# Performance work log

Measured on AMD Instinct MI355X. Metric: run time of the kernel, lower is better.

## Reference

```python
import jax, jax.numpy as jnp
import numpy as np

L, D, H, DH, DI, V, S, B = 12, 768, 12, 64, 3072, 32000, 512, 2
LN_EPS = 1e-3  # keras LayerNormalization default epsilon

def _gelu(x):
    return x * 0.5 * (1.0 + jnp.tanh(np.sqrt(2.0 / np.pi).astype(np.float32) * (x + 0.044715 * x ** 3)))

def _layer_norm(x, g, b):
    mu = jnp.mean(x, axis=-1, keepdims=True)
    var = jnp.mean((x - mu) ** 2, axis=-1, keepdims=True)
    return (x - mu) * jax.lax.rsqrt(var + LN_EPS) * g + b

def _rel_shift(x, klen):
    # x: [qlen, rlen, b, n] -> shifted [qlen, klen, b, n]
    q, r, b, n = x.shape
    x = x.reshape(r, q, b, n)[1:].reshape(q, r - 1, b, n)
    return x[:, :klen]

def _pos_emb():
    # relative positions klen..-qlen+1 (attn_type='bi', mems=None -> klen=qlen=S)
    pos_seq = jnp.arange(S, -S, -1.0, dtype=jnp.float32)                      # [2S]
    inv_freq = 1.0 / (10000.0 ** (jnp.arange(0, D, 2, dtype=jnp.float32) / D))
    sinusoid = pos_seq[:, None] * inv_freq[None, :]
    pe = jnp.concatenate([jnp.sin(sinusoid), jnp.cos(sinusoid)], axis=-1)     # [2S, D]
    return jnp.broadcast_to(pe[:, None, :], (2 * S, B, D))                    # [2S, B, D]

def setup_inputs() -> dict:
    key = jax.random.key(0)
    ks = jax.random.split(key, 12)
    rn = lambda k, sh: 0.02 * jax.random.normal(k, sh, dtype=jnp.float32)
    return {
        "inp_k": jax.random.randint(ks[0], (S, B), 0, V),
        "seg_ids": jax.random.randint(ks[1], (S, B), 0, 2),
        "input_mask": jax.random.randint(ks[2], (S, B), 0, 2),
        "lookup_table": rn(ks[3], (V, D)),
        "Wq": rn(ks[4], (L, D, H, DH)),
        "Wk": rn(ks[5], (L, D, H, DH)),
        "Wv": rn(ks[6], (L, D, H, DH)),
        "Wr": rn(ks[7], (L, D, H, DH)),
        "Wo": rn(ks[8], (L, D, H, DH)),
        "r_w_bias": rn(ks[9], (L, H, DH)),
        "r_r_bias": rn(ks[10], (L, H, DH)),
        "r_s_bias": rn(ks[11], (L, H, DH)),
        "seg_embed": rn(jax.random.fold_in(key, 100), (L, 2, H, DH)),
        "ln_attn_g": jnp.ones((L, D), jnp.float32),
        "ln_attn_b": jnp.zeros((L, D), jnp.float32),
        "ln_ff_g": jnp.ones((L, D), jnp.float32),
        "ln_ff_b": jnp.zeros((L, D), jnp.float32),
        "ff_w1": rn(jax.random.fold_in(key, 101), (L, D, DI)),
        "ff_b1": jnp.zeros((L, DI), jnp.float32),
        "ff_w2": rn(jax.random.fold_in(key, 102), (L, DI, D)),
        "ff_b2": jnp.zeros((L, D), jnp.float32),
    }

def reference(inp_k, seg_ids, input_mask, lookup_table, Wq, Wk, Wv, Wr, Wo,
              r_w_bias, r_r_bias, r_s_bias, seg_embed,
              ln_attn_g, ln_attn_b, ln_ff_g, ln_ff_b,
              ff_w1, ff_b1, ff_w2, ff_b2):
    h = lookup_table[inp_k]                                                   # [S,B,D]
    r = _pos_emb()                                                            # [2S,B,D]
    # segment "same/different" one-hot matrix [q,k,b,2]
    seg_mat = jax.nn.one_hot((seg_ids[:, None, :] != seg_ids[None, :, :]).astype(jnp.int32), 2, dtype=jnp.float32)
    attn_mask = input_mask.astype(jnp.float32)[None, :, :, None]              # [1,S,B,1] broadcast over q,heads
    scale = DH ** -0.5
    for l in range(L):
        q = jnp.einsum('ibh,hnd->ibnd', h, Wq[l])
        k = jnp.einsum('ibh,hnd->ibnd', h, Wk[l])
        v = jnp.einsum('ibh,hnd->ibnd', h, Wv[l])
        kr = jnp.einsum('ibh,hnd->ibnd', r, Wr[l])                            # [2S,B,n,d]
        ac = jnp.einsum('ibnd,jbnd->ijbn', q + r_w_bias[l], k)
        bd = _rel_shift(jnp.einsum('ibnd,jbnd->ijbn', q + r_r_bias[l], kr), S)
        ef = jnp.einsum('ibnd,snd->ibns', q + r_s_bias[l], seg_embed[l])
        ef = jnp.einsum('ijbs,ibns->ijbn', seg_mat, ef)
        score = (ac + bd + ef) * scale - 1e30 * attn_mask
        prob = jax.nn.softmax(score, axis=1)                                  # softmax over key axis j
        vec = jnp.einsum('ijbn,jbnd->ibnd', prob, v)
        h = _layer_norm(jnp.einsum('ibnd,hnd->ibh', vec, Wo[l]) + h, ln_attn_g[l], ln_attn_b[l])
        ff = _gelu(jnp.einsum('ibd,df->ibf', h, ff_w1[l]) + ff_b1[l])
        ff = jnp.einsum('ibf,fd->ibd', ff, ff_w2[l]) + ff_b2[l]
        h = _layer_norm(ff + h, ln_ff_g[l], ln_ff_b[l])
    return h
```

## Files before the change

kernel.cpp:

```cpp
#include <hip/hip_runtime.h>
#include <hip/hip_bf16.h>
#include <math.h>

#define S 512
#define B 2
#define D 768
#define H 12
#define DH 64
#define DI 3072
#define NL 12
#define NTOK (S * B)

typedef __attribute__((ext_vector_type(8))) short short8v;
typedef __attribute__((ext_vector_type(4))) float f32x4;

__device__ __forceinline__ unsigned short f2b(float f) {
  union { float f; unsigned int u; } v; v.f = f;
  unsigned int r = v.u + 0x7fffu + ((v.u >> 16) & 1u);
  return (unsigned short)(r >> 16);
}
__device__ __forceinline__ float b2f(unsigned short u) {
  union { unsigned int u; float f; } v; v.u = ((unsigned int)u) << 16;
  return v.f;
}

__device__ __forceinline__ float gelu_f(float x) {
  const float c = 0.7978845608028654f;
  float t = tanhf(c * (x + 0.044715f * x * x * x));
  return x * 0.5f * (1.0f + t);
}

__device__ __forceinline__ int vkey(int r) {
  return ((((r & 7) ^ ((r >> 3) & 7)) & 7) << 3);
}

__global__ __launch_bounds__(256) void embed_kernel(const int* __restrict__ inp_k,
                                                    const float* __restrict__ lut,
                                                    float* __restrict__ h,
                                                    unsigned short* __restrict__ h_bf) {
  int t = blockIdx.x;
  int id = inp_k[t];
  for (int j = threadIdx.x; j < D; j += 256) {
    float v = lut[(size_t)id * D + j];
    h[t * D + j] = v;
    h_bf[t * D + j] = f2b(v);
  }
}

__global__ __launch_bounds__(384) void posemb_kernel(unsigned short* __restrict__ r2b) {
  int j = blockIdx.x;
  int d = threadIdx.x;
  float pos = (float)(S - j);
  float inv_freq = expf(-logf(10000.0f) * (2.0f * (float)d / (float)D));
  float x = pos * inv_freq;
  r2b[j * D + d]       = f2b(sinf(x));
  r2b[j * D + 384 + d] = f2b(cosf(x));
}

__device__ __forceinline__ void transpose_swz(const float* __restrict__ src,
                                              unsigned short* __restrict__ dst,
                                              int K, int N, int tile, int n_base,
                                              float* __restrict__ Ls ) {
  int ntk = K >> 6;
  int tk = tile % ntk, tn = tile / ntk;
  int k0 = tk << 6, n0 = tn << 6;
  int tid = threadIdx.x;
  int rr = tid >> 4, c4 = (tid & 15) * 4;
#pragma unroll
  for (int r = 0; r < 4; ++r) {
    int k = rr + r * 16;
    float4 a = *(const float4*)&src[(size_t)(k0 + k) * N + n0 + c4];
    Ls[(c4 + 0) * 65 + k] = a.x;
    Ls[(c4 + 1) * 65 + k] = a.y;
    Ls[(c4 + 2) * 65 + k] = a.z;
    Ls[(c4 + 3) * 65 + k] = a.w;
  }
  __syncthreads();
  int nl = tid >> 2, kc0 = (tid & 3) << 4;
  float f[16];
#pragma unroll
  for (int c = 0; c < 16; ++c) f[c] = Ls[nl * 65 + kc0 + c];
  short8v v0, v1;
#pragma unroll
  for (int e = 0; e < 8; ++e) {
    v0[e] = (short)f2b(f[e]);
    v1[e] = (short)f2b(f[8 + e]);
  }
  int ng = n_base + n0;
  size_t tilebase = ((size_t)(ng >> 7) * ntk + tk) * 8192;
  int row = (ng & 64) + nl;
  int key = (row & 7) << 3;
  *(short8v*)&dst[tilebase + row * 64 + (kc0 ^ key)] = v0;
  *(short8v*)&dst[tilebase + row * 64 + ((kc0 + 8) ^ key)] = v1;
}

__global__ __launch_bounds__(256) void prep_all(const float* __restrict__ Wq,
                                                const float* __restrict__ Wk,
                                                const float* __restrict__ Wv,
                                                const float* __restrict__ Wr,
                                                const float* __restrict__ Wo,
                                                const float* __restrict__ W1,
                                                const float* __restrict__ W2,
                                                unsigned short* __restrict__ wqkv_t,
                                                unsigned short* __restrict__ wr_t,
                                                unsigned short* __restrict__ wo_t,
                                                unsigned short* __restrict__ w1_t,
                                                unsigned short* __restrict__ w2_t) {
  __shared__ float Ls[64 * 65];
  const size_t DD = (size_t)D * D;
  const size_t DDI = (size_t)D * DI;
  int tb = blockIdx.x;
  int l = tb / 1872, t2 = tb % 1872;
  int tid = threadIdx.x;
  if (t2 < 432) {
    int which = t2 / 144, tile = t2 % 144;
    const float* src = (which == 0 ? Wq : (which == 1 ? Wk : Wv)) + l * DD;
    transpose_swz(src, wqkv_t + l * 3 * DD, D, D, tile, which * D, Ls);
  } else if (t2 < 576) {
    transpose_swz(Wr + l * DD, wr_t + l * DD, D, D, t2 - 432, 0, Ls);
  } else if (t2 < 1152) {
    transpose_swz(W1 + l * DDI, w1_t + l * DDI, D, DI, t2 - 576, 0, Ls);
  } else if (t2 < 1728) {
    transpose_swz(W2 + l * DDI, w2_t + l * DDI, DI, D, t2 - 1152, 0, Ls);
  } else {
    int c = t2 - 1728;
    int tkk = c % 12, tnn = c / 12;
    int k0 = tkk << 6, n0 = tnn << 6;
    int nl = tid >> 2, kc0 = (tid & 3) << 4;
    const float* srcp = Wo + l * DD + (size_t)(n0 + nl) * D + k0 + kc0;
    float4 a0 = *(const float4*)&srcp[0];
    float4 a1 = *(const float4*)&srcp[4];
    float4 a2 = *(const float4*)&srcp[8];
    float4 a3 = *(const float4*)&srcp[12];
    short8v v0, v1;
    v0[0] = (short)f2b(a0.x); v0[1] = (short)f2b(a0.y); v0[2] = (short)f2b(a0.z); v0[3] = (short)f2b(a0.w);
    v0[4] = (short)f2b(a1.x); v0[5] = (short)f2b(a1.y); v0[6] = (short)f2b(a1.z); v0[7] = (short)f2b(a1.w);
    v1[0] = (short)f2b(a2.x); v1[1] = (short)f2b(a2.y); v1[2] = (short)f2b(a2.z); v1[3] = (short)f2b(a2.w);
    v1[4] = (short)f2b(a3.x); v1[5] = (short)f2b(a3.y); v1[6] = (short)f2b(a3.z); v1[7] = (short)f2b(a3.w);
    unsigned short* dst = wo_t + l * DD;
    size_t tilebase = ((size_t)(n0 >> 7) * 12 + tkk) * 8192;
    int row = (n0 & 64) + nl;
    int key = (row & 7) << 3;
    *(short8v*)&dst[tilebase + row * 64 + (kc0 ^ key)] = v0;
    *(short8v*)&dst[tilebase + row * 64 + ((kc0 + 8) ^ key)] = v1;
  }
}

template <int ACT, int OUTBF>
__device__ __forceinline__ void gemm_tile(const unsigned short* __restrict__ A,
                                          const unsigned short* __restrict__ Wt,
                                          const float* __restrict__ bias,
                                          float* __restrict__ Cf,
                                          unsigned short* __restrict__ Cb,
                                          int N, int K, int bm, int bn,
                                          int kbeg, int kend) {
  __shared__ __align__(16) unsigned short As[64 * 64];
  __shared__ __align__(16) unsigned short Bs[128 * 64];
  const int tid = threadIdx.x, lane = tid & 63, w = tid >> 6;
  const int l8 = lane >> 3, lm8 = lane & 7;
  const int aColByte = ((lm8 ^ l8) << 4);
  const int KT = K >> 6;
  const size_t wtn = (size_t)(bn >> 7) * KT;

  f32x4 acc[4][2];
#pragma unroll
  for (int mi = 0; mi < 4; ++mi)
#pragma unroll
    for (int ni = 0; ni < 2; ++ni)
      acc[mi][ni] = (f32x4){0.f, 0.f, 0.f, 0.f};

  for (int kt = kbeg; kt < kend; kt += 64) {
    __syncthreads();
#pragma unroll
    for (int c = 0; c < 2; ++c) {
      int row = c * 32 + w * 8 + l8;
      const char* src = (const char*)&A[(size_t)(bm + row) * K + kt] + aColByte;
      __builtin_amdgcn_global_load_lds(
          (const __attribute__((address_space(1))) void*)src,
          (__attribute__((address_space(3))) void*)((char*)As + c * 4096 + w * 1024),
          16, 0, 0);
    }
    const char* wt = (const char*)&Wt[(wtn + (kt >> 6)) * 8192];
#pragma unroll
    for (int c = 0; c < 4; ++c) {
      __builtin_amdgcn_global_load_lds(
          (const __attribute__((address_space(1))) void*)(wt + c * 4096 + w * 1024 + lane * 16),
          (__attribute__((address_space(3))) void*)((char*)Bs + c * 4096 + w * 1024),
          16, 0, 0);
    }
    __syncthreads();
#pragma unroll
    for (int ks = 0; ks < 2; ++ks) {
      const int kus = ks * 32 + (lane >> 4) * 8;
      short8v af[4], bf[2];
#pragma unroll
      for (int mi = 0; mi < 4; ++mi) {
        int row = mi * 16 + (lane & 15);
        af[mi] = *(const short8v*)&As[row * 64 + (kus ^ ((row & 7) << 3))];
      }
#pragma unroll
      for (int ni = 0; ni < 2; ++ni) {
        int row = w * 32 + ni * 16 + (lane & 15);
        bf[ni] = *(const short8v*)&Bs[row * 64 + (kus ^ ((row & 7) << 3))];
      }
#pragma unroll
      for (int mi = 0; mi < 4; ++mi)
#pragma unroll
        for (int ni = 0; ni < 2; ++ni)
          acc[mi][ni] = __builtin_amdgcn_mfma_f32_16x16x32_bf16(af[mi], bf[ni], acc[mi][ni], 0, 0, 0);
    }
  }

  int r0 = (lane >> 4) * 4, cc = lane & 15;
#pragma unroll
  for (int mi = 0; mi < 4; ++mi) {
    int row = bm + mi * 16 + r0;
#pragma unroll
    for (int ni = 0; ni < 2; ++ni) {
      int col = bn + w * 32 + ni * 16 + cc;
      float bv = bias ? bias[col] : 0.0f;
#pragma unroll
      for (int r = 0; r < 4; ++r) {
        float v = acc[mi][ni][r] + bv;
        if (ACT == 1) v = gelu_f(v);
        if (OUTBF) Cb[(size_t)(row + r) * N + col] = f2b(v);
        else       Cf[(size_t)(row + r) * N + col] = v;
      }
    }
  }
}

__global__ __launch_bounds__(256) void gemm_qkv(const unsigned short* __restrict__ h_bf,
                                                const unsigned short* __restrict__ wqkv,
                                                unsigned short* __restrict__ qkv_bf) {
  int bx = blockIdx.x;
  gemm_tile<0, 1>(h_bf, wqkv, nullptr, nullptr, qkv_bf, 2304, 768,
                  (bx / 18) * 64, (bx % 18) * 128, 0, 768);
}

__global__ __launch_bounds__(256) void gemm_kr_all(const unsigned short* __restrict__ r2_bf,
                                                   const unsigned short* __restrict__ wr_t,
                                                   unsigned short* __restrict__ kr_all) {
  int bx = blockIdx.x;
  int l = bx / 96, b2 = bx % 96;
  gemm_tile<0, 1>(r2_bf, wr_t + (size_t)l * D * D, nullptr, nullptr,
                  kr_all + (size_t)l * NTOK * D, 768, 768,
                  (b2 / 6) * 64, (b2 % 6) * 128, 0, 768);
}

template <int ACT>
__global__ __launch_bounds__(256) void gemm_bias(const unsigned short* __restrict__ A,
                                                 const unsigned short* __restrict__ W,
                                                 const float* __restrict__ bias,
                                                 unsigned short* __restrict__ C,
                                                 int N, int K, int ncb) {
  int bx = blockIdx.x;
  gemm_tile<ACT, 1>(A, W, bias, nullptr, C, N, K, (bx / ncb) * 64, (bx % ncb) * 128, 0, K);
}

__global__ __launch_bounds__(256) void gemm_splitk(const unsigned short* __restrict__ A,
                                                   const unsigned short* __restrict__ W,
                                                   float* __restrict__ part,
                                                   int N, int K, int kch) {
  int kz = blockIdx.z;
  float* Cf = part + (size_t)kz * NTOK * N;
  gemm_tile<0, 0>(A, W, nullptr, Cf, nullptr, N, K,
                  blockIdx.y * 64, blockIdx.x * 128, kz * kch, (kz + 1) * kch);
}

__global__ __launch_bounds__(256) void attn_kernel(const unsigned short* __restrict__ qkv,
                                                   const unsigned short* __restrict__ krb,
                                                   const int* __restrict__ seg_ids,
                                                   const int* __restrict__ input_mask,
                                                   const float* __restrict__ rwb,
                                                   const float* __restrict__ rrb,
                                                   const float* __restrict__ rsb,
                                                   const float* __restrict__ segemb,
                                                   unsigned short* __restrict__ vec_bf) {
  __shared__ __align__(16) char smem[51840];
  unsigned short* qw_s = (unsigned short*)(smem + 0);
  unsigned short* qr_s = (unsigned short*)(smem + 4608);
  unsigned short* k_s  = (unsigned short*)(smem + 9216);
  unsigned short* kr_s = (unsigned short*)(smem + 18432);
  unsigned short* bd_s = (unsigned short*)(smem + 32256);
  unsigned short* vt_s = (unsigned short*)(smem + 38912);
  unsigned short* pb_s = (unsigned short*)(smem + 47104);
  float* sc_s  = (float*)(smem + 9216);
  float* efs    = (float*)(smem + 51200);
  float* frow_s = (float*)(smem + 51456);
  float* rinv_s = (float*)(smem + 51584);
  int*   segrow = (int*)(smem + 51712);

  const int it = blockIdx.x * 32, b = blockIdx.y, n = blockIdx.z;
  const int tid = threadIdx.x, lane = tid & 63, w = tid >> 6;

  {
    int il = tid >> 3, d8 = (tid & 7) * 8;
    int t = (it + il) * B + b;
    short8v q0 = *(const short8v*)&qkv[(size_t)t * 2304 + n * 64 + d8];
    short8v ow0, or0;
#pragma unroll
    for (int e = 0; e < 8; ++e) {
      float f0 = b2f((unsigned short)q0[e]);
      ow0[e] = (short)f2b(f0 + rwb[n * 64 + d8 + e]);
      or0[e] = (short)f2b(f0 + rrb[n * 64 + d8 + e]);
    }
    *(short8v*)&qw_s[il * 72 + d8] = ow0;
    *(short8v*)&qr_s[il * 72 + d8] = or0;
  }
  if (tid < 64) {
    int il = tid >> 1, s = tid & 1;
    int t = (it + il) * B + b;
    float acc = 0.0f;
    for (int d = 0; d < 64; ++d)
      acc = fmaf(b2f(qkv[(size_t)t * 2304 + n * 64 + d]) + rsb[n * 64 + d],
                 segemb[(s * H + n) * 64 + d], acc);
    efs[s * 32 + il] = acc;
  }
  if (tid < 32) segrow[tid] = seg_ids[(it + tid) * B + b];

  {
#pragma unroll
    for (int c = 0; c < 2; ++c) {
      int idx = tid + c * 256;
      int row = idx >> 3, k8 = (idx & 7) * 8;
      *(short8v*)&k_s[row * 72 + k8] =
          *(const short8v*)&qkv[(size_t)(row * B + b) * 2304 + 768 + n * 64 + k8];
    }
    int u0 = 481 - it;
#pragma unroll
    for (int c = 0; c < 3; ++c) {
      int idx = tid + c * 256;
      int row = idx >> 3, k8 = (idx & 7) * 8;
      *(short8v*)&kr_s[row * 72 + k8] =
          *(const short8v*)&krb[(size_t)(u0 + row) * 768 + n * 64 + k8];
    }
  }

  f32x4 acc_v[2];
  acc_v[0] = (f32x4){0.f, 0.f, 0.f, 0.f};
  acc_v[1] = (f32x4){0.f, 0.f, 0.f, 0.f};
  float m_run = -3.0e38f;
  float rsq = 0.0f;
  const int srow = tid >> 3, sc0 = (tid & 7) * 8;

  __syncthreads();

  for (int jt = 0; jt < 512; jt += 64) {
    const int vj = tid >> 2, vd16 = (tid & 3) * 16;
    short8v vl0 = *(const short8v*)&qkv[(size_t)((jt + vj) * B + b) * 2304 + 1536 + n * 64 + vd16];
    short8v vl1 = *(const short8v*)&qkv[(size_t)((jt + vj) * B + b) * 2304 + 1536 + n * 64 + vd16 + 8];

    f32x4 jacc[3][2];
#pragma unroll
    for (int t = 0; t < 3; ++t) {
      jacc[t][0] = (f32x4){0.f, 0.f, 0.f, 0.f};
      jacc[t][1] = (f32x4){0.f, 0.f, 0.f, 0.f};
    }
#pragma unroll
    for (int ks = 0; ks < 2; ++ks) {
      int kb = ks * 32 + (lane >> 4) * 8;
      short8v aw[2], ar[2];
#pragma unroll
      for (int mi = 0; mi < 2; ++mi) {
        aw[mi] = *(const short8v*)&qw_s[(mi * 16 + (lane & 15)) * 72 + kb];
        ar[mi] = *(const short8v*)&qr_s[(mi * 16 + (lane & 15)) * 72 + kb];
      }
      {
        short8v bk = *(const short8v*)&k_s[(w * 16 + (lane & 15)) * 72 + kb];
        jacc[0][0] = __builtin_amdgcn_mfma_f32_16x16x32_bf16(aw[0], bk, jacc[0][0], 0, 0, 0);
        jacc[0][1] = __builtin_amdgcn_mfma_f32_16x16x32_bf16(aw[1], bk, jacc[0][1], 0, 0, 0);
      }
      {
        short8v br = *(const short8v*)&kr_s[(w * 16 + (lane & 15)) * 72 + kb];
        jacc[1][0] = __builtin_amdgcn_mfma_f32_16x16x32_bf16(ar[0], br, jacc[1][0], 0, 0, 0);
        jacc[1][1] = __builtin_amdgcn_mfma_f32_16x16x32_bf16(ar[1], br, jacc[1][1], 0, 0, 0);
      }
      if (w < 2) {
        short8v br = *(const short8v*)&kr_s[((w + 4) * 16 + (lane & 15)) * 72 + kb];
        jacc[2][0] = __builtin_amdgcn_mfma_f32_16x16x32_bf16(ar[0], br, jacc[2][0], 0, 0, 0);
        jacc[2][1] = __builtin_amdgcn_mfma_f32_16x16x32_bf16(ar[1], br, jacc[2][1], 0, 0, 0);
      }
    }
#pragma unroll
    for (int t = 1; t < 3; ++t) {
      int cf = w + (t - 1) * 4;
      if (t == 1 || w < 2) {
#pragma unroll
        for (int mi = 0; mi < 2; ++mi)
#pragma unroll
          for (int r = 0; r < 4; ++r)
            bd_s[(mi * 16 + (lane >> 4) * 4 + r) * 104 + cf * 16 + (lane & 15)] =
                f2b(jacc[t][mi][r]);
      }
    }
    __syncthreads();

    {
      int jl = w * 16 + (lane & 15);
      int jg = jt + jl;
      float maskterm = -1e30f * (float)input_mask[jg * B + b];
      int segj = seg_ids[jg * B + b];
#pragma unroll
      for (int mi = 0; mi < 2; ++mi)
#pragma unroll
        for (int r = 0; r < 4; ++r) {
          int il = mi * 16 + (lane >> 4) * 4 + r;
          float bd = b2f(bd_s[il * 104 + 31 - il + jl]);
          float e = efs[(segrow[il] != segj ? 1 : 0) * 32 + il];
          sc_s[il * 68 + jl] = (jacc[0][mi][r] + bd + e) * 0.125f + maskterm;
        }
    }
    __syncthreads();

    {
      float4 f0 = *(const float4*)&sc_s[srow * 68 + sc0];
      float4 f1 = *(const float4*)&sc_s[srow * 68 + sc0 + 4];
      float mx = fmaxf(fmaxf(fmaxf(f0.x, f0.y), fmaxf(f0.z, f0.w)),
                       fmaxf(fmaxf(f1.x, f1.y), fmaxf(f1.z, f1.w)));
      mx = fmaxf(mx, __shfl_xor(mx, 1, 8));
      mx = fmaxf(mx, __shfl_xor(mx, 2, 8));
      mx = fmaxf(mx, __shfl_xor(mx, 4, 8));
      float mnew = fmaxf(m_run, mx);
      float fsc = __expf(m_run - mnew);
      m_run = mnew;
      float p0 = __expf(f0.x - mnew), p1 = __expf(f0.y - mnew);
      float p2 = __expf(f0.z - mnew), p3 = __expf(f0.w - mnew);
      float p4 = __expf(f1.x - mnew), p5 = __expf(f1.y - mnew);
      float p6 = __expf(f1.z - mnew), p7 = __expf(f1.w - mnew);
      rsq = rsq * fsc + ((p0 + p1 + p2 + p3) + (p4 + p5 + p6 + p7));
      short8v o0;
      o0[0] = (short)f2b(p0); o0[1] = (short)f2b(p1); o0[2] = (short)f2b(p2); o0[3] = (short)f2b(p3);
      o0[4] = (short)f2b(p4); o0[5] = (short)f2b(p5); o0[6] = (short)f2b(p6); o0[7] = (short)f2b(p7);
      *(short8v*)&pb_s[srow * 64 + (sc0 ^ vkey(srow))] = o0;
      if ((tid & 7) == 0) frow_s[srow] = fsc;
#pragma unroll
      for (int e = 0; e < 8; ++e) {
        int d0 = vd16 + e, d1 = vd16 + 8 + e;
        vt_s[d0 * 64 + (vj ^ vkey(d0))] = (unsigned short)vl0[e];
        vt_s[d1 * 64 + (vj ^ vkey(d1))] = (unsigned short)vl1[e];
      }
    }
    __syncthreads();

#pragma unroll
    for (int mi = 0; mi < 2; ++mi) {
#pragma unroll
      for (int r = 0; r < 4; ++r)
        acc_v[mi][r] *= frow_s[mi * 16 + (lane >> 4) * 4 + r];
    }
#pragma unroll
    for (int ks = 0; ks < 2; ++ks) {
      int kb = ks * 32 + (lane >> 4) * 8;
      int vrow = w * 16 + (lane & 15);
      short8v bv = *(const short8v*)&vt_s[vrow * 64 + (kb ^ vkey(vrow))];
#pragma unroll
      for (int mi = 0; mi < 2; ++mi) {
        int prow = mi * 16 + (lane & 15);
        short8v ap = *(const short8v*)&pb_s[prow * 64 + (kb ^ vkey(prow))];
        acc_v[mi] = __builtin_amdgcn_mfma_f32_16x16x32_bf16(ap, bv, acc_v[mi], 0, 0, 0);
      }
    }
    if (jt < 448) {
      int jn = jt + 64;
#pragma unroll
      for (int c = 0; c < 2; ++c) {
        int idx = tid + c * 256;
        int row = idx >> 3, k8 = (idx & 7) * 8;
        *(short8v*)&k_s[row * 72 + k8] =
            *(const short8v*)&qkv[(size_t)((jn + row) * B + b) * 2304 + 768 + n * 64 + k8];
      }
      int u0 = 481 - it + jn;
#pragma unroll
      for (int c = 0; c < 3; ++c) {
        int idx = tid + c * 256;
        int row = idx >> 3, k8 = (idx & 7) * 8;
        *(short8v*)&kr_s[row * 72 + k8] =
            *(const short8v*)&krb[(size_t)(u0 + row) * 768 + n * 64 + k8];
      }
    }
    __syncthreads();
  }

  {
    float tot = rsq;
    tot += __shfl_xor(tot, 1, 8);
    tot += __shfl_xor(tot, 2, 8);
    tot += __shfl_xor(tot, 4, 8);
    if ((tid & 7) == 0) rinv_s[srow] = 1.0f / tot;
  }
  __syncthreads();

#pragma unroll
  for (int mi = 0; mi < 2; ++mi)
#pragma unroll
    for (int r = 0; r < 4; ++r) {
      int row = mi * 16 + (lane >> 4) * 4 + r;
      int d = w * 16 + (lane & 15);
      int t = (it + row) * B + b;
      vec_bf[(size_t)t * D + n * 64 + d] = f2b(acc_v[mi][r] * rinv_s[row]);
    }
}

template <int P, int HASBIAS>
__global__ __launch_bounds__(256) void add_ln_reduce(const float* __restrict__ part,
                                                     const float* __restrict__ bias,
                                                     float* __restrict__ h,
                                                     unsigned short* __restrict__ h_bf,
                                                     const float* __restrict__ g,
                                                     const float* __restrict__ bi) {
  int t = blockIdx.x;
  int tid = threadIdx.x;
  int wv = tid >> 6, lane = tid & 63;
  __shared__ float red[8];
  float vx = 0.f, vy = 0.f, vz = 0.f, vw = 0.f;
  float s = 0.0f;
  int c = tid * 4;
  if (tid < 192) {
    float4 x = {0.f, 0.f, 0.f, 0.f};
#pragma unroll
    for (int p = 0; p < P; ++p) {
      float4 pp = *(const float4*)&part[(size_t)p * NTOK * D + (size_t)t * D + c];
      x.x += pp.x; x.y += pp.y; x.z += pp.z; x.w += pp.w;
    }
    if (HASBIAS) {
      float4 bb = *(const float4*)&bias[c];
      x.x += bb.x; x.y += bb.y; x.z += bb.z; x.w += bb.w;
    }
    float4 hh = *(const float4*)&h[(size_t)t * D + c];
    vx = x.x + hh.x; vy = x.y + hh.y; vz = x.z + hh.z; vw = x.w + hh.w;
    s = vx + vy + vz + vw;
  }
#pragma unroll
  for (int m = 1; m < 64; m <<= 1) s += __shfl_xor(s, m, 64);
  if (lane == 0) red[wv] = s;
  __syncthreads();
  float mu = (red[0] + red[1] + red[2] + red[3]) * (1.0f / (float)D);
  float s2 = 0.0f;
  if (tid < 192) {
    float dx = vx - mu, dy = vy - mu, dz = vz - mu, dw = vw - mu;
    s2 = dx * dx + dy * dy + dz * dz + dw * dw;
  }
#pragma unroll
  for (int m = 1; m < 64; m <<= 1) s2 += __shfl_xor(s2, m, 64);
  if (lane == 0) red[4 + wv] = s2;
  __syncthreads();
  float var = (red[4] + red[5] + red[6] + red[7]) * (1.0f / (float)D);
  float rstd = rsqrtf(var + 1e-3f);
  if (tid < 192) {
    float4 gg = *(const float4*)&g[c];
    float4 bb = *(const float4*)&bi[c];
    float o0 = (vx - mu) * rstd * gg.x + bb.x;
    float o1 = (vy - mu) * rstd * gg.y + bb.y;
    float o2 = (vz - mu) * rstd * gg.z + bb.z;
    float o3 = (vw - mu) * rstd * gg.w + bb.w;
    float4 of = {o0, o1, o2, o3};
    *(float4*)&h[(size_t)t * D + c] = of;
    ushort4 ob;
    ob.x = f2b(o0); ob.y = f2b(o1); ob.z = f2b(o2); ob.w = f2b(o3);
    *(ushort4*)&h_bf[(size_t)t * D + c] = ob;
  }
}

extern "C" void kernel_launch(void* const* d_in, const int* in_sizes, int n_in,
                              void* d_out, int out_size, void* d_ws, size_t ws_size,
                              hipStream_t stream) {
  const int*   inp_k      = (const int*)d_in[0];
  const int*   seg_ids    = (const int*)d_in[1];
  const int*   input_mask = (const int*)d_in[2];
  const float* lut        = (const float*)d_in[3];
  const float* Wq         = (const float*)d_in[4];
  const float* Wk         = (const float*)d_in[5];
  const float* Wv         = (const float*)d_in[6];
  const float* Wr         = (const float*)d_in[7];
  const float* Wo         = (const float*)d_in[8];
  const float* r_w_bias   = (const float*)d_in[9];
  const float* r_r_bias   = (const float*)d_in[10];
  const float* r_s_bias   = (const float*)d_in[11];
  const float* seg_embed  = (const float*)d_in[12];
  const float* ln_attn_g  = (const float*)d_in[13];
  const float* ln_attn_b  = (const float*)d_in[14];
  const float* ln_ff_g    = (const float*)d_in[15];
  const float* ln_ff_b    = (const float*)d_in[16];
  const float* ff_w1      = (const float*)d_in[17];
  const float* ff_b1      = (const float*)d_in[18];
  const float* ff_w2      = (const float*)d_in[19];
  const float* ff_b2      = (const float*)d_in[20];

  float* h = (float*)d_out;
  char* wp = (char*)d_ws;
  auto alloc = [&](size_t bytes) -> void* {
    void* p = (void*)wp;
    wp += (bytes + 255) & ~(size_t)255;
    return p;
  };
  const size_t TOKD = (size_t)NTOK * D;
  const size_t DD = (size_t)D * D;
  const size_t DDI = (size_t)D * DI;
  unsigned short* qkv_bf = (unsigned short*)alloc((size_t)NTOK * 2304 * 2);
  unsigned short* kr_all = (unsigned short*)alloc((size_t)NL * TOKD * 2);
  unsigned short* h_bf   = (unsigned short*)alloc(TOKD * 2);
  unsigned short* r2_bf  = (unsigned short*)alloc(TOKD * 2);
  unsigned short* vec_bf = (unsigned short*)alloc(TOKD * 2);
  unsigned short* ff1_bf = (unsigned short*)alloc((size_t)NTOK * DI * 2);
  float* part = (float*)alloc((size_t)4 * TOKD * 4);
  unsigned short* wqkv_t = (unsigned short*)alloc((size_t)NL * 3 * DD * 2);
  unsigned short* wr_t   = (unsigned short*)alloc((size_t)NL * DD * 2);
  unsigned short* wo_t   = (unsigned short*)alloc((size_t)NL * DD * 2);
  unsigned short* w1_t   = (unsigned short*)alloc((size_t)NL * DDI * 2);
  unsigned short* w2_t   = (unsigned short*)alloc((size_t)NL * DDI * 2);

  prep_all<<<NL * 1872, 256, 0, stream>>>(Wq, Wk, Wv, Wr, Wo, ff_w1, ff_w2,
                                          wqkv_t, wr_t, wo_t, w1_t, w2_t);
  embed_kernel<<<NTOK, 256, 0, stream>>>(inp_k, lut, h, h_bf);
  posemb_kernel<<<2 * S, 384, 0, stream>>>(r2_bf);
  gemm_kr_all<<<NL * 96, 256, 0, stream>>>(r2_bf, wr_t, kr_all);

  for (int l = 0; l < NL; ++l) {
    gemm_qkv<<<288, 256, 0, stream>>>(h_bf, wqkv_t + (size_t)l * 3 * DD, qkv_bf);

    attn_kernel<<<dim3(16, B, H), 256, 0, stream>>>(
        qkv_bf, kr_all + (size_t)l * TOKD, seg_ids, input_mask,
        r_w_bias + (size_t)l * D, r_r_bias + (size_t)l * D,
        r_s_bias + (size_t)l * D, seg_embed + (size_t)l * 2 * H * DH,
        vec_bf);

    gemm_splitk<<<dim3(6, 16, 2), 256, 0, stream>>>(
        vec_bf, wo_t + (size_t)l * DD, part, D, D, 384);
    add_ln_reduce<2, 0><<<NTOK, 256, 0, stream>>>(
        part, nullptr, h, h_bf, ln_attn_g + (size_t)l * D, ln_attn_b + (size_t)l * D);

    gemm_bias<1><<<24 * 16, 256, 0, stream>>>(
        h_bf, w1_t + (size_t)l * DDI, ff_b1 + (size_t)l * DI, ff1_bf, DI, D, 24);

    gemm_splitk<<<dim3(6, 16, 4), 256, 0, stream>>>(
        ff1_bf, w2_t + (size_t)l * DDI, part, D, DI, 768);
    add_ln_reduce<4, 1><<<NTOK, 256, 0, stream>>>(
        part, ff_b2 + (size_t)l * D, h, h_bf, ln_ff_g + (size_t)l * D, ln_ff_b + (size_t)l * D);
  }
}
```

Before: 1.285 ms.

## Load attention K/Kr tiles directly to LDS with XOR swizzle; retune FF2 split-k

Replaces the register-staged global-to-shared copies of the K and relative-position K tiles in the attention kernel with direct global_load_lds transfers. The padded stride-72 layout becomes an unpadded stride-64 layout with an XOR swizzle so the MFMA operand reads still avoid LDS bank conflicts, and the shared-memory footprint shrinks. The FF2 split-k GEMM also drops from 4 to 3 K-splits, with the matching reduce template changed. Risks include relying on the compiler to place waits correctly for the async LDS loads before the barrier, and reduced parallelism in the FF2 GEMM.

```diff
diff --git a/kernel.cpp b/kernel.cpp
--- a/kernel.cpp
+++ b/kernel.cpp
@@ -277,22 +277,25 @@
                                                    const float* __restrict__ rsb,
                                                    const float* __restrict__ segemb,
                                                    unsigned short* __restrict__ vec_bf) {
-  __shared__ __align__(16) char smem[51840];
+  __shared__ __align__(16) char smem[49280];
   unsigned short* qw_s = (unsigned short*)(smem + 0);
   unsigned short* qr_s = (unsigned short*)(smem + 4608);
   unsigned short* k_s  = (unsigned short*)(smem + 9216);
-  unsigned short* kr_s = (unsigned short*)(smem + 18432);
-  unsigned short* bd_s = (unsigned short*)(smem + 32256);
-  unsigned short* vt_s = (unsigned short*)(smem + 38912);
-  unsigned short* pb_s = (unsigned short*)(smem + 47104);
+  unsigned short* kr_s = (unsigned short*)(smem + 17408);
+  unsigned short* bd_s = (unsigned short*)(smem + 29696);
+  unsigned short* vt_s = (unsigned short*)(smem + 36352);
+  unsigned short* pb_s = (unsigned short*)(smem + 44544);
   float* sc_s  = (float*)(smem + 9216);
-  float* efs    = (float*)(smem + 51200);
-  float* frow_s = (float*)(smem + 51456);
-  float* rinv_s = (float*)(smem + 51584);
-  int*   segrow = (int*)(smem + 51712);
+  float* efs    = (float*)(smem + 48640);
+  float* frow_s = (float*)(smem + 48896);
+  float* rinv_s = (float*)(smem + 49024);
+  int*   segrow = (int*)(smem + 49152);
 
   const int it = blockIdx.x * 32, b = blockIdx.y, n = blockIdx.z;
   const int tid = threadIdx.x, lane = tid & 63, w = tid >> 6;
+  const int l8 = lane >> 3, lm8 = lane & 7;
+  const int aColByte = ((lm8 ^ l8) << 4);
+  const int rdkey = ((lane & 7) << 3);
 
   {
     int il = tid >> 3, d8 = (tid & 7) * 8;
@@ -322,18 +325,22 @@
   {
 #pragma unroll
     for (int c = 0; c < 2; ++c) {
-      int idx = tid + c * 256;
-      int row = idx >> 3, k8 = (idx & 7) * 8;
-      *(short8v*)&k_s[row * 72 + k8] =
-          *(const short8v*)&qkv[(size_t)(row * B + b) * 2304 + 768 + n * 64 + k8];
+      int row = c * 32 + w * 8 + l8;
+      const char* src = (const char*)&qkv[(size_t)(row * B + b) * 2304 + 768 + n * 64] + aColByte;
+      __builtin_amdgcn_global_load_lds(
+          (const __attribute__((address_space(1))) void*)src,
+          (__attribute__((address_space(3))) void*)((char*)k_s + c * 4096 + w * 1024),
+          16, 0, 0);
     }
     int u0 = 481 - it;
 #pragma unroll
     for (int c = 0; c < 3; ++c) {
-      int idx = tid + c * 256;
-      int row = idx >> 3, k8 = (idx & 7) * 8;
-      *(short8v*)&kr_s[row * 72 + k8] =
-          *(const short8v*)&krb[(size_t)(u0 + row) * 768 + n * 64 + k8];
+      int row = c * 32 + w * 8 + l8;
+      const char* src = (const char*)&krb[(size_t)(u0 + row) * 768 + n * 64] + aColByte;
+      __builtin_amdgcn_global_load_lds(
+          (const __attribute__((address_space(1))) void*)src,
+          (__attribute__((address_space(3))) void*)((char*)kr_s + c * 4096 + w * 1024),
+          16, 0, 0);
     }
   }
 
@@ -360,6 +367,7 @@
 #pragma unroll
     for (int ks = 0; ks < 2; ++ks) {
       int kb = ks * 32 + (lane >> 4) * 8;
+      int kk = kb ^ rdkey;
       short8v aw[2], ar[2];
 #pragma unroll
       for (int mi = 0; mi < 2; ++mi) {
@@ -367,17 +375,17 @@
         ar[mi] = *(const short8v*)&qr_s[(mi * 16 + (lane & 15)) * 72 + kb];
       }
       {
-        short8v bk = *(const short8v*)&k_s[(w * 16 + (lane & 15)) * 72 + kb];
+        short8v bk = *(const short8v*)&k_s[(w * 16 + (lane & 15)) * 64 + kk];
         jacc[0][0] = __builtin_amdgcn_mfma_f32_16x16x32_bf16(aw[0], bk, jacc[0][0], 0, 0, 0);
         jacc[0][1] = __builtin_amdgcn_mfma_f32_16x16x32_bf16(aw[1], bk, jacc[0][1], 0, 0, 0);
       }
       {
-        short8v br = *(const short8v*)&kr_s[(w * 16 + (lane & 15)) * 72 + kb];
+        short8v br = *(const short8v*)&kr_s[(w * 16 + (lane & 15)) * 64 + kk];
         jacc[1][0] = __builtin_amdgcn_mfma_f32_16x16x32_bf16(ar[0], br, jacc[1][0], 0, 0, 0);
         jacc[1][1] = __builtin_amdgcn_mfma_f32_16x16x32_bf16(ar[1], br, jacc[1][1], 0, 0, 0);
       }
       if (w < 2) {
-        short8v br = *(const short8v*)&kr_s[((w + 4) * 16 + (lane & 15)) * 72 + kb];
+        short8v br = *(const short8v*)&kr_s[((w + 4) * 16 + (lane & 15)) * 64 + kk];
         jacc[2][0] = __builtin_amdgcn_mfma_f32_16x16x32_bf16(ar[0], br, jacc[2][0], 0, 0, 0);
         jacc[2][1] = __builtin_amdgcn_mfma_f32_16x16x32_bf16(ar[1], br, jacc[2][1], 0, 0, 0);
       }
@@ -465,18 +473,22 @@
       int jn = jt + 64;
 #pragma unroll
       for (int c = 0; c < 2; ++c) {
-        int idx = tid + c * 256;
-        int row = idx >> 3, k8 = (idx & 7) * 8;
-        *(short8v*)&k_s[row * 72 + k8] =
-            *(const short8v*)&qkv[(size_t)((jn + row) * B + b) * 2304 + 768 + n * 64 + k8];
+        int row = c * 32 + w * 8 + l8;
+        const char* src = (const char*)&qkv[(size_t)((jn + row) * B + b) * 2304 + 768 + n * 64] + aColByte;
+        __builtin_amdgcn_global_load_lds(
+            (const __attribute__((address_space(1))) void*)src,
+            (__attribute__((address_space(3))) void*)((char*)k_s + c * 4096 + w * 1024),
+            16, 0, 0);
       }
       int u0 = 481 - it + jn;
 #pragma unroll
       for (int c = 0; c < 3; ++c) {
-        int idx = tid + c * 256;
-        int row = idx >> 3, k8 = (idx & 7) * 8;
-        *(short8v*)&kr_s[row * 72 + k8] =
-            *(const short8v*)&krb[(size_t)(u0 + row) * 768 + n * 64 + k8];
+        int row = c * 32 + w * 8 + l8;
+        const char* src = (const char*)&krb[(size_t)(u0 + row) * 768 + n * 64] + aColByte;
+        __builtin_amdgcn_global_load_lds(
+            (const __attribute__((address_space(1))) void*)src,
+            (__attribute__((address_space(3))) void*)((char*)kr_s + c * 4096 + w * 1024),
+            16, 0, 0);
       }
     }
     __syncthreads();
@@ -633,9 +645,9 @@
     gemm_bias<1><<<24 * 16, 256, 0, stream>>>(
         h_bf, w1_t + (size_t)l * DDI, ff_b1 + (size_t)l * DI, ff1_bf, DI, D, 24);
 
-    gemm_splitk<<<dim3(6, 16, 4), 256, 0, stream>>>(
-        ff1_bf, w2_t + (size_t)l * DDI, part, D, DI, 768);
-    add_ln_reduce<4, 1><<<NTOK, 256, 0, stream>>>(
+    gemm_splitk<<<dim3(6, 16, 3), 256, 0, stream>>>(
+        ff1_bf, w2_t + (size_t)l * DDI, part, D, DI, 1024);
+    add_ln_reduce<3, 1><<<NTOK, 256, 0, stream>>>(
         part, ff_b2 + (size_t)l * D, h, h_bf, ln_ff_g + (size_t)l * D, ln_ff_b + (size_t)l * D);
   }
 }
```

After: 1.314 ms. +2.2%, slower.
